# Performance work log

Measured on AMD Instinct MI355X. Metric: run time of the kernel, lower is better.

Reference implementation:

```python
import jax, jax.numpy as jnp
from jax import lax
import numpy as np


def setup_inputs() -> dict:
    key = jax.random.key(0)
    ks = jax.random.split(key, 5)
    B = 256
    data = jax.random.normal(ks[0], (B, 1, 28, 28), jnp.float32)
    # ConvLayer: Conv2d(1->256, k=9, s=1)
    w1 = jax.random.normal(ks[1], (256, 1, 9, 9), jnp.float32) * 0.1
    b1 = jnp.zeros((256,), jnp.float32)
    # PrimaryCaps: Conv2d(256->256, k=9, s=2)
    w2 = jax.random.normal(ks[2], (256, 256, 9, 9), jnp.float32) * 0.02
    b2 = jnp.zeros((256,), jnp.float32)
    # DigitCaps routing weights: (in_caps=1152, out_caps=10, out_len=16, in_len=8)
    W = jax.random.normal(ks[3], (1152, 10, 16, 8), jnp.float32) * 0.05
    return {"data": data, "w1": w1, "b1": b1, "w2": w2, "b2": b2, "W": W}


def _squash(s):
    # s: (B,1,10,16); sn*s / ((1+sn)*sqrt(sn)) as in the torch code
    sn = jnp.sum(s * s, axis=-1, keepdims=True)
    return sn * s / ((1.0 + sn) * jnp.sqrt(sn))


def reference(data, w1, b1, w2, b2, W):
    # ConvLayer: conv k9 s1 VALID + relu -> (B,256,20,20)
    x = lax.conv(data, w1, (1, 1), 'VALID') + b1[None, :, None, None]
    x = jax.nn.relu(x)
    # PrimaryCaps: conv k9 s2 VALID -> (B,256,6,6)
    x = lax.conv(x, w2, (2, 2), 'VALID') + b2[None, :, None, None]
    B = x.shape[0]
    # toCapsules: (B,256,6,6) -> (B,8,32,6,6) -> (B,8,1152) -> (B,1152,8)
    x = x.reshape(B, 8, -1).transpose(0, 2, 1)
    # u_hat[b,n,o,k] = W[n,o,k,d] @ x[b,n,d]  -> (B,1152,10,16)
    u_hat = jnp.einsum('nokd,bnd->bnok', W, x)
    b_ij = jnp.zeros((B, 1152, 10, 1), u_hat.dtype)
    num_iterations = 3
    v_j = None
    for it in range(1, num_iterations + 1):
        c_ij = jax.nn.softmax(b_ij, axis=1)            # over input capsules
        s_j = jnp.sum(c_ij * u_hat, axis=1, keepdims=True)  # (B,1,10,16)
        v_j = _squash(s_j)
        if it < num_iterations:
            # Faithful to the torch code: a_ij = u_hat * sum_k(v_j), broadcast
            # over input capsules; b_ij widens to (B,1152,10,16) after iter 1.
            a_ij = u_hat * jnp.sum(v_j, axis=-1, keepdims=True)
            b_ij = b_ij + a_ij
    return v_j[:, 0]  # (B,10,16)
```

## Files before the change

### kernel.cpp

```cpp
#include <hip/hip_runtime.h>
#include <hip/hip_bf16.h>
#include <cmath>


typedef float f32x4 __attribute__((ext_vector_type(4)));
typedef short s16x8 __attribute__((ext_vector_type(8)));
typedef unsigned int u32;

static __device__ __forceinline__ short f2bf(float x) {
  __hip_bfloat16 h = __float2bfloat16(x);
  return *reinterpret_cast<short*>(&h);
}
static __device__ __forceinline__ float bf2f(short s) {
  __hip_bfloat16 h;
  *reinterpret_cast<short*>(&h) = s;
  return __bfloat162float(h);
}
static __device__ __forceinline__ void stage16(const short* g, short* l) {
  __builtin_amdgcn_global_load_lds(
      (const __attribute__((address_space(1))) u32*)(const void*)g,
      (__attribute__((address_space(3))) u32*)(void*)l, 16, 0, 0);
}

#define CHUNK_SHORTS 23552
#define ODD_OFS 12288

__global__ __launch_bounds__(256) void prep_all(
    const float* __restrict__ w2, s16x8* __restrict__ wstg,
    const float* __restrict__ data, const float* __restrict__ w1,
    const float* __restrict__ b1, short* __restrict__ c1g) {
  __shared__ float sbuf[12784];
  const int t = threadIdx.x;
  if (blockIdx.x < 512) {
    const int b = blockIdx.x;
    const int chunk = b >> 6;
    const int kg = (b >> 4) & 3;
    const int cot = b & 15;
    const int co0 = cot * 16;
    const size_t gbase = (size_t)(chunk * 32 + kg * 8) * 81;
    for (int i = t; i < 10368; i += 256) {
      const int r = i / 648, e = i - r * 648;
      sbuf[i] = w2[(size_t)(co0 + r) * 20736 + gbase + e];
    }
    __syncthreads();
    for (int p = t; p < 1296; p += 256) {
      const int tap = p >> 4, co = p & 15;
      s16x8 hi, lo;
#pragma unroll
      for (int i = 0; i < 8; ++i) {
        const float x = sbuf[co * 648 + i * 81 + tap];
        const short h = f2bf(x);
        hi[i] = h;
        lo[i] = f2bf(x - bf2f(h));
      }
      const size_t T = (size_t)(chunk * 81 + tap);
      wstg[T * 2048 + kg * 256 + co0 + co] = hi;
      wstg[T * 2048 + 1024 + kg * 256 + co0 + co] = lo;
    }
    return;
  }
  const int cb = blockIdx.x - 512;
  const int img = cb >> 1;
  const int chh = cb & 1;
  float* simg = sbuf;
  short* c1buf = (short*)&sbuf[1008];
  for (int i = t; i < 784; i += 256)
    simg[(i / 28) * 36 + (i % 28)] = data[img * 784 + i];
  __syncthreads();
  for (int cc = 0; cc < 4; ++cc) {
    const int chunk = chh * 4 + cc;
    for (int task = t; task < 608; task += 256) {
      const int ci = task & 31;
      const int y = task >> 5;
      const int ch = chunk * 32 + ci;
      const float* wr = w1 + ch * 81;
      float acc[20];
      const float bz = b1[ch];
#pragma unroll
      for (int x = 0; x < 20; ++x) acc[x] = bz;
#pragma unroll
      for (int ky = 0; ky < 9; ++ky) {
        float rr[28];
#pragma unroll
        for (int q = 0; q < 7; ++q)
          *(float4*)&rr[q * 4] = *(const float4*)&simg[(y + ky) * 36 + q * 4];
#pragma unroll
        for (int kx = 0; kx < 9; ++kx) {
          const float w = wr[ky * 9 + kx];
#pragma unroll
          for (int x = 0; x < 20; ++x) acc[x] = fmaf(w, rr[x + kx], acc[x]);
        }
      }
      const int kg = ci >> 3, il = ci & 7;
#pragma unroll
      for (int x = 0; x < 19; ++x) {
        const int xh = x >> 1;
        const int r = (x & 1) ? (y * 9 + xh) : (y * 10 + xh);
        short* base = c1buf + ((x & 1) ? ODD_OFS : 0);
        const float v = fmaxf(acc[x], 0.f);
        const short hi = f2bf(v);
        const short lo = f2bf(v - bf2f(hi));
        base[r * 64 + (((kg + r) & 7) << 3) + il] = hi;
        base[r * 64 + (((kg + 4 + r) & 7) << 3) + il] = lo;
      }
    }
    __syncthreads();
    {
      s16x8* dst = (s16x8*)(c1g + (size_t)(img * 8 + chunk) * CHUNK_SHORTS);
      const s16x8* srcb = (const s16x8*)c1buf;
      for (int i = t; i < 2944; i += 256) dst[i] = srcb[i];
    }
    __syncthreads();
  }
}

__global__ __launch_bounds__(256) void conv2_mfma(
    const short* __restrict__ c1g, const short* __restrict__ wstg,
    const float* __restrict__ b2, float* __restrict__ xcaps0,
    float* __restrict__ xcaps1) {
  const int t = threadIdx.x;
  const int bid = blockIdx.x;
  const int xcd = bid & 7;
  const int ksp = xcd & 1;
  const int coh = (xcd >> 1) & 1;
  const int img = (bid >> 3) * 2 + (xcd >> 2);
  const int lane = t & 63;
  const int wv = t >> 6;
  const int r16 = lane & 15;
  const int kg = lane >> 4;

  __shared__ short c1[12288];

  int arowE[3], arowO[3];
#pragma unroll
  for (int m = 0; m < 3; ++m) {
    int pos = m * 16 + r16;
    if (pos > 35) pos = 35;
    const int oy = pos / 6, ox = pos % 6;
    arowE[m] = oy * 20 + ox;
    arowO[m] = oy * 18 + ox;
  }
  int bOff[2], con[2];
  float bias[2];
#pragma unroll
  for (int j = 0; j < 2; ++j) {
    const int co = coh * 128 + wv * 32 + j * 16 + r16;
    con[j] = co;
    bOff[j] = kg * 256 + co;
    bias[j] = (ksp == 0) ? b2[co] : 0.f;
  }
  float* xcp = (ksp == 0) ? xcaps0 : xcaps1;

  const f32x4 vzero = {0.f, 0.f, 0.f, 0.f};
  f32x4 acc[3][2];
#pragma unroll
  for (int m = 0; m < 3; ++m)
#pragma unroll
    for (int j = 0; j < 2; ++j) acc[m][j] = vzero;

  const s16x8* wsv = (const s16x8*)wstg;

  for (int cc = 0; cc < 4; ++cc) {
    const int chunk = ksp * 4 + cc;
    const short* src = c1g + (size_t)(img * 8 + chunk) * CHUNK_SHORTS;
    const size_t bb = (size_t)chunk * 81 * 2048;

    __syncthreads();
    for (int c = wv; c < 24; c += 4)
      stage16(src + c * 512 + lane * 8, &c1[c * 512]);
    __syncthreads();
    {
      s16x8 BHc[2], BLc[2];
#pragma unroll
      for (int j = 0; j < 2; ++j) {
        BHc[j] = wsv[bb + bOff[j]];
        BLc[j] = wsv[bb + bOff[j] + 1024];
      }
      for (int ky = 0; ky < 9; ++ky) {
#pragma unroll
        for (int kxi = 0; kxi < 5; ++kxi) {
          s16x8 BHn[2], BLn[2];
          if (!(ky == 8 && kxi == 4)) {
            const int nky = (kxi == 4) ? ky + 1 : ky;
            const int nkxi = (kxi == 4) ? 0 : kxi + 1;
            const size_t nb = bb + (size_t)(nky * 9 + 2 * nkxi) * 2048;
#pragma unroll
            for (int j = 0; j < 2; ++j) {
              BHn[j] = wsv[nb + bOff[j]];
              BLn[j] = wsv[nb + bOff[j] + 1024];
            }
          }
          s16x8 AH[3], AL[3];
#pragma unroll
          for (int m = 0; m < 3; ++m) {
            const int r = arowE[m] + ky * 10 + kxi;
            AH[m] = *(const s16x8*)&c1[r * 64 + (((kg + r) & 7) << 3)];
            AL[m] = *(const s16x8*)&c1[r * 64 + (((kg + 4 + r) & 7) << 3)];
          }
#pragma unroll
          for (int m = 0; m < 3; ++m)
#pragma unroll
            for (int j = 0; j < 2; ++j)
              acc[m][j] = __builtin_amdgcn_mfma_f32_16x16x32_bf16(AH[m], BHc[j], acc[m][j], 0, 0, 0);
#pragma unroll
          for (int m = 0; m < 3; ++m)
#pragma unroll
            for (int j = 0; j < 2; ++j)
              acc[m][j] = __builtin_amdgcn_mfma_f32_16x16x32_bf16(AL[m], BHc[j], acc[m][j], 0, 0, 0);
#pragma unroll
          for (int m = 0; m < 3; ++m)
#pragma unroll
            for (int j = 0; j < 2; ++j)
              acc[m][j] = __builtin_amdgcn_mfma_f32_16x16x32_bf16(AH[m], BLc[j], acc[m][j], 0, 0, 0);
#pragma unroll
          for (int j = 0; j < 2; ++j) { BHc[j] = BHn[j]; BLc[j] = BLn[j]; }
        }
      }
    }

    __syncthreads();
    for (int c = wv; c < 22; c += 4)
      stage16(src + ODD_OFS + c * 512 + lane * 8, &c1[c * 512]);
    __syncthreads();
    {
      s16x8 BHc[2], BLc[2];
#pragma unroll
      for (int j = 0; j < 2; ++j) {
        BHc[j] = wsv[bb + 2048 + bOff[j]];
        BLc[j] = wsv[bb + 2048 + bOff[j] + 1024];
      }
      for (int ky = 0; ky < 9; ++ky) {
#pragma unroll
        for (int kxi = 0; kxi < 4; ++kxi) {
          s16x8 BHn[2], BLn[2];
          if (!(ky == 8 && kxi == 3)) {
            const int nky = (kxi == 3) ? ky + 1 : ky;
            const int nkxi = (kxi == 3) ? 0 : kxi + 1;
            const size_t nb = bb + (size_t)(nky * 9 + 2 * nkxi + 1) * 2048;
#pragma unroll
            for (int j = 0; j < 2; ++j) {
              BHn[j] = wsv[nb + bOff[j]];
              BLn[j] = wsv[nb + bOff[j] + 1024];
            }
          }
          s16x8 AH[3], AL[3];
#pragma unroll
          for (int m = 0; m < 3; ++m) {
            const int r = arowO[m] + ky * 9 + kxi;
            AH[m] = *(const s16x8*)&c1[r * 64 + (((kg + r) & 7) << 3)];
            AL[m] = *(const s16x8*)&c1[r * 64 + (((kg + 4 + r) & 7) << 3)];
          }
#pragma unroll
          for (int m = 0; m < 3; ++m)
#pragma unroll
            for (int j = 0; j < 2; ++j)
              acc[m][j] = __builtin_amdgcn_mfma_f32_16x16x32_bf16(AH[m], BHc[j], acc[m][j], 0, 0, 0);
#pragma unroll
          for (int m = 0; m < 3; ++m)
#pragma unroll
            for (int j = 0; j < 2; ++j)
              acc[m][j] = __builtin_amdgcn_mfma_f32_16x16x32_bf16(AL[m], BHc[j], acc[m][j], 0, 0, 0);
#pragma unroll
          for (int m = 0; m < 3; ++m)
#pragma unroll
            for (int j = 0; j < 2; ++j)
              acc[m][j] = __builtin_amdgcn_mfma_f32_16x16x32_bf16(AH[m], BLc[j], acc[m][j], 0, 0, 0);
#pragma unroll
          for (int j = 0; j < 2; ++j) { BHc[j] = BHn[j]; BLc[j] = BLn[j]; }
        }
      }
    }
  }

#pragma unroll
  for (int m = 0; m < 3; ++m) {
#pragma unroll
    for (int jj = 0; jj < 4; ++jj) {
      const int pos = m * 16 + kg * 4 + jj;
      if (pos < 36) {
#pragma unroll
        for (int j = 0; j < 2; ++j) {
          const int co = con[j];
          const int n = (co & 31) * 36 + pos;
          xcp[((size_t)img * 1152 + n) * 8 + (co >> 5)] = acc[m][j][jj] + bias[j];
        }
      }
    }
  }
}

__global__ __launch_bounds__(256) void routing_fused(const float* __restrict__ xcaps0,
                                                     const float* __restrict__ xcaps1,
                                                     const float* __restrict__ W,
                                                     float* __restrict__ out) {
  const int o = blockIdx.x >> 7;
  const int bp = blockIdx.x & 127;
  const int b0 = bp * 2, b1 = b0 + 1;
  const int t = threadIdx.x;
  const int k = t & 15, ng = t >> 4;
  __shared__ float xs0[1152 * 8];
  __shared__ float xs1[1152 * 8];
  __shared__ double redA[256], redB[256], redC[256], redD[256];
  __shared__ float s0s[16], s1s[16];
  __shared__ float sv0, sv1;
  __shared__ double f0, f1;

  {
    const float4* p00 = (const float4*)(xcaps0 + (size_t)b0 * 9216);
    const float4* p01 = (const float4*)(xcaps1 + (size_t)b0 * 9216);
    const float4* p10 = (const float4*)(xcaps0 + (size_t)b1 * 9216);
    const float4* p11 = (const float4*)(xcaps1 + (size_t)b1 * 9216);
    float4* d0 = (float4*)xs0;
    float4* d1 = (float4*)xs1;
    for (int i = t; i < 2304; i += 256) {
      float4 a = p00[i], b = p01[i];
      float4 c = p10[i], d = p11[i];
      float4 s0, s1;
      s0.x = a.x + b.x; s0.y = a.y + b.y; s0.z = a.z + b.z; s0.w = a.w + b.w;
      s1.x = c.x + d.x; s1.y = c.y + d.y; s1.z = c.z + d.z; s1.w = c.w + d.w;
      d0[i] = s0;
      d1[i] = s1;
    }
  }
  __syncthreads();

  const int n0 = ng * 72;
  float u0[72], u1[72];
  const float* wp = W + ((size_t)(n0 * 10 + o) * 16 + k) * 8;
#pragma unroll
  for (int i = 0; i < 72; ++i) {
    const float* wq = wp + (size_t)i * 1280;
    const float4 wa = *(const float4*)wq;
    const float4 wb = *(const float4*)(wq + 4);
    const float4 xa0 = *(const float4*)&xs0[(n0 + i) * 8];
    const float4 xb0 = *(const float4*)&xs0[(n0 + i) * 8 + 4];
    const float4 xa1 = *(const float4*)&xs1[(n0 + i) * 8];
    const float4 xb1 = *(const float4*)&xs1[(n0 + i) * 8 + 4];
    float s0 = wa.x * xa0.x + wa.y * xa0.y + wa.z * xa0.z + wa.w * xa0.w
             + wb.x * xb0.x + wb.y * xb0.y + wb.z * xb0.z + wb.w * xb0.w;
    float s1 = wa.x * xa1.x + wa.y * xa1.y + wa.z * xa1.z + wa.w * xa1.w
             + wb.x * xb1.x + wb.y * xb1.y + wb.z * xb1.z + wb.w * xb1.w;
    u0[i] = s0;
    u1[i] = s1;
  }

  {
    double S0 = 0.0, S1 = 0.0;
#pragma unroll
    for (int i = 0; i < 72; ++i) { S0 += (double)u0[i]; S1 += (double)u1[i]; }
    redA[t] = S0; redB[t] = S1;
  }
  __syncthreads();
  if (t < 16) {
    double t0 = 0.0, t1 = 0.0;
#pragma unroll
    for (int g = 0; g < 16; ++g) { t0 += redA[g * 16 + t]; t1 += redB[g * 16 + t]; }
    s0s[t] = (float)(t0 * (double)(1.0f / 1152.0f));
    s1s[t] = (float)(t1 * (double)(1.0f / 1152.0f));
  }
  __syncthreads();
  if (t == 0) {
    double sn = 0.0;
#pragma unroll
    for (int kk = 0; kk < 16; ++kk) sn += (double)s0s[kk] * (double)s0s[kk];
    double f = sn / ((1.0 + sn) * sqrt(sn));
    double sv = 0.0;
#pragma unroll
    for (int kk = 0; kk < 16; ++kk) sv += (double)s0s[kk] * f;
    sv0 = (float)sv;
    sn = 0.0;
#pragma unroll
    for (int kk = 0; kk < 16; ++kk) sn += (double)s1s[kk] * (double)s1s[kk];
    f = sn / ((1.0 + sn) * sqrt(sn));
    sv = 0.0;
#pragma unroll
    for (int kk = 0; kk < 16; ++kk) sv += (double)s1s[kk] * f;
    sv1 = (float)sv;
  }
  __syncthreads();
  const float v10 = sv0, v11 = sv1;

  {
    double E0 = 0.0, EU0 = 0.0, E1 = 0.0, EU1 = 0.0;
#pragma unroll
    for (int i = 0; i < 72; ++i) {
      const float e0 = expf(u0[i] * v10);
      E0 += (double)e0;
      EU0 += (double)e0 * (double)u0[i];
      const float e1 = expf(u1[i] * v11);
      E1 += (double)e1;
      EU1 += (double)e1 * (double)u1[i];
    }
    redA[t] = E0; redB[t] = EU0; redC[t] = E1; redD[t] = EU1;
  }
  __syncthreads();
  if (t < 16) {
    double e0 = 0.0, s0 = 0.0, e1 = 0.0, s1 = 0.0;
#pragma unroll
    for (int g = 0; g < 16; ++g) {
      e0 += redA[g * 16 + t]; s0 += redB[g * 16 + t];
      e1 += redC[g * 16 + t]; s1 += redD[g * 16 + t];
    }
    s0s[t] = (float)(s0 / e0);
    s1s[t] = (float)(s1 / e1);
  }
  __syncthreads();
  if (t == 0) {
    double sn = 0.0;
#pragma unroll
    for (int kk = 0; kk < 16; ++kk) sn += (double)s0s[kk] * (double)s0s[kk];
    double f = sn / ((1.0 + sn) * sqrt(sn));
    double sv = 0.0;
#pragma unroll
    for (int kk = 0; kk < 16; ++kk) sv += (double)s0s[kk] * f;
    sv0 = v10 + (float)sv;
    sn = 0.0;
#pragma unroll
    for (int kk = 0; kk < 16; ++kk) sn += (double)s1s[kk] * (double)s1s[kk];
    f = sn / ((1.0 + sn) * sqrt(sn));
    sv = 0.0;
#pragma unroll
    for (int kk = 0; kk < 16; ++kk) sv += (double)s1s[kk] * f;
    sv1 = v11 + (float)sv;
  }
  __syncthreads();
  const float v20 = sv0, v21 = sv1;

  {
    double E0 = 0.0, EU0 = 0.0, E1 = 0.0, EU1 = 0.0;
#pragma unroll
    for (int i = 0; i < 72; ++i) {
      const float e0 = expf(u0[i] * v20);
      E0 += (double)e0;
      EU0 += (double)e0 * (double)u0[i];
      const float e1 = expf(u1[i] * v21);
      E1 += (double)e1;
      EU1 += (double)e1 * (double)u1[i];
    }
    redA[t] = E0; redB[t] = EU0; redC[t] = E1; redD[t] = EU1;
  }
  __syncthreads();
  if (t < 16) {
    double e0 = 0.0, s0 = 0.0, e1 = 0.0, s1 = 0.0;
#pragma unroll
    for (int g = 0; g < 16; ++g) {
      e0 += redA[g * 16 + t]; s0 += redB[g * 16 + t];
      e1 += redC[g * 16 + t]; s1 += redD[g * 16 + t];
    }
    s0s[t] = (float)(s0 / e0);
    s1s[t] = (float)(s1 / e1);
  }
  __syncthreads();
  if (t == 0) {
    double sn = 0.0;
#pragma unroll
    for (int kk = 0; kk < 16; ++kk) sn += (double)s0s[kk] * (double)s0s[kk];
    f0 = sn / ((1.0 + sn) * sqrt(sn));
    sn = 0.0;
#pragma unroll
    for (int kk = 0; kk < 16; ++kk) sn += (double)s1s[kk] * (double)s1s[kk];
    f1 = sn / ((1.0 + sn) * sqrt(sn));
  }
  __syncthreads();
  if (t < 16) {
    out[b0 * 160 + o * 16 + t] = (float)((double)s0s[t] * f0);
    out[b1 * 160 + o * 16 + t] = (float)((double)s1s[t] * f1);
  }
}

extern "C" void kernel_launch(void* const* d_in, const int* in_sizes, int n_in,
                              void* d_out, int out_size, void* d_ws, size_t ws_size,
                              hipStream_t stream) {
  const float* data = (const float*)d_in[0];
  const float* w1   = (const float*)d_in[1];
  const float* b1   = (const float*)d_in[2];
  const float* w2   = (const float*)d_in[3];
  const float* b2   = (const float*)d_in[4];
  const float* W    = (const float*)d_in[5];
  float* out = (float*)d_out;

  short* wstg   = (short*)d_ws;
  short* c1g    = wstg + 10616832;
  float* xcaps0 = (float*)(c1g + 48234496);
  float* xcaps1 = xcaps0 + 2359296;

  prep_all<<<1024, 256, 0, stream>>>(w2, (s16x8*)wstg, data, w1, b1, c1g);
  conv2_mfma<<<1024, 256, 0, stream>>>(c1g, wstg, b2, xcaps0, xcaps1);
  routing_fused<<<1280, 256, 0, stream>>>(xcaps0, xcaps1, W, out);
}
```

Measured before the change: 528.7 us.

## Split conv2 reduction four ways across blocks and sum partials in routing

```diff
diff --git a/kernel.cpp b/kernel.cpp
--- a/kernel.cpp
+++ b/kernel.cpp
@@ -116,14 +116,13 @@
 
 __global__ __launch_bounds__(256) void conv2_mfma(
     const short* __restrict__ c1g, const short* __restrict__ wstg,
-    const float* __restrict__ b2, float* __restrict__ xcaps0,
-    float* __restrict__ xcaps1) {
+    const float* __restrict__ b2, float* __restrict__ xcaps) {
   const int t = threadIdx.x;
   const int bid = blockIdx.x;
   const int xcd = bid & 7;
-  const int ksp = xcd & 1;
-  const int coh = (xcd >> 1) & 1;
-  const int img = (bid >> 3) * 2 + (xcd >> 2);
+  const int ksp = xcd & 3;
+  const int coh = xcd >> 2;
+  const int img = bid >> 3;
   const int lane = t & 63;
   const int wv = t >> 6;
   const int r16 = lane & 15;
@@ -149,7 +148,7 @@
     bOff[j] = kg * 256 + co;
     bias[j] = (ksp == 0) ? b2[co] : 0.f;
   }
-  float* xcp = (ksp == 0) ? xcaps0 : xcaps1;
+  float* xcp = xcaps + (size_t)ksp * 2359296;
 
   const f32x4 vzero = {0.f, 0.f, 0.f, 0.f};
   f32x4 acc[3][2];
@@ -160,8 +159,8 @@
 
   const s16x8* wsv = (const s16x8*)wstg;
 
-  for (int cc = 0; cc < 4; ++cc) {
-    const int chunk = ksp * 4 + cc;
+  for (int cc = 0; cc < 2; ++cc) {
+    const int chunk = ksp * 2 + cc;
     const short* src = c1g + (size_t)(img * 8 + chunk) * CHUNK_SHORTS;
     const size_t bb = (size_t)chunk * 81 * 2048;
 
@@ -289,8 +288,7 @@
   }
 }
 
-__global__ __launch_bounds__(256) void routing_fused(const float* __restrict__ xcaps0,
-                                                     const float* __restrict__ xcaps1,
+__global__ __launch_bounds__(256) void routing_fused(const float* __restrict__ xcaps,
                                                      const float* __restrict__ W,
                                                      float* __restrict__ out) {
   const int o = blockIdx.x >> 7;
@@ -306,18 +304,17 @@
   __shared__ double f0, f1;
 
   {
-    const float4* p00 = (const float4*)(xcaps0 + (size_t)b0 * 9216);
-    const float4* p01 = (const float4*)(xcaps1 + (size_t)b0 * 9216);
-    const float4* p10 = (const float4*)(xcaps0 + (size_t)b1 * 9216);
-    const float4* p11 = (const float4*)(xcaps1 + (size_t)b1 * 9216);
     float4* d0 = (float4*)xs0;
     float4* d1 = (float4*)xs1;
     for (int i = t; i < 2304; i += 256) {
-      float4 a = p00[i], b = p01[i];
-      float4 c = p10[i], d = p11[i];
-      float4 s0, s1;
-      s0.x = a.x + b.x; s0.y = a.y + b.y; s0.z = a.z + b.z; s0.w = a.w + b.w;
-      s1.x = c.x + d.x; s1.y = c.y + d.y; s1.z = c.z + d.z; s1.w = c.w + d.w;
+      float4 s0 = {0.f, 0.f, 0.f, 0.f}, s1 = {0.f, 0.f, 0.f, 0.f};
+#pragma unroll
+      for (int p = 0; p < 4; ++p) {
+        const float4 a = ((const float4*)(xcaps + (size_t)p * 2359296 + (size_t)b0 * 9216))[i];
+        const float4 c = ((const float4*)(xcaps + (size_t)p * 2359296 + (size_t)b1 * 9216))[i];
+        s0.x += a.x; s0.y += a.y; s0.z += a.z; s0.w += a.w;
+        s1.x += c.x; s1.y += c.y; s1.z += c.z; s1.w += c.w;
+      }
       d0[i] = s0;
       d1[i] = s1;
     }
@@ -479,12 +476,11 @@
   const float* W    = (const float*)d_in[5];
   float* out = (float*)d_out;
 
-  short* wstg   = (short*)d_ws;
-  short* c1g    = wstg + 10616832;
-  float* xcaps0 = (float*)(c1g + 48234496);
-  float* xcaps1 = xcaps0 + 2359296;
+  short* wstg  = (short*)d_ws;
+  short* c1g   = wstg + 10616832;
+  float* xcaps = (float*)(c1g + 48234496);
 
   prep_all<<<1024, 256, 0, stream>>>(w2, (s16x8*)wstg, data, w1, b1, c1g);
-  conv2_mfma<<<1024, 256, 0, stream>>>(c1g, wstg, b2, xcaps0, xcaps1);
-  routing_fused<<<1280, 256, 0, stream>>>(xcaps0, xcaps1, W, out);
-}
+  conv2_mfma<<<2048, 256, 0, stream>>>(c1g, wstg, b2, xcaps);
+  routing_fused<<<1280, 256, 0, stream>>>(xcaps, W, out);
+}
```

New measurement: 547.3 us. 3.5% more time.
